# Kernel optimization log

Measured on AMD Instinct MI355X. Metric: run time of the kernel, lower is better.

## Reference

```python
import jax, jax.numpy as jnp
import numpy as np

# Forest of complete binary trees modeling query plans.
B = 512          # number of plans (trees)
D = 11           # tree depth; leaves at level D-1
LEAVES = 1 << (D - 1)      # 1024 leaves per tree
N_INT = LEAVES - 1         # 1023 internal nodes per tree (BFS heap order)
F_LEAF = 64      # leaf ('Scan') feature dim
F_INT = 32       # internal operator feature dim
H = 128          # hidden_dim
NHID = 4         # num_layers=5 -> input layer + 4 hidden layers
DV = 32          # data_vec_dim
OUT = 1 + DV     # latency + data vector


def _mlp(x, W_in, b_in, W_hid, b_hid, W_out, b_out):
    """GenericUnit: Linear+ReLU input layer, NHID Linear+ReLU hidden layers, linear output."""
    h = jax.nn.relu(x @ W_in + b_in)
    for i in range(W_hid.shape[0]):  # small fixed loop over layers
        h = jax.nn.relu(h @ W_hid[i] + b_hid[i])
    return h @ W_out + b_out


def setup_inputs() -> dict:
    key = jax.random.key(0)
    ks = jax.random.split(key, 8)

    def w(k, shape, fan_in):
        return jax.random.normal(k, shape, jnp.float32) * np.float32(1.0 / np.sqrt(fan_in))

    return {
        "leaf_feat": jax.random.normal(ks[0], (B, LEAVES, F_LEAF), jnp.float32),
        "int_feat": jax.random.normal(ks[1], (B, N_INT, F_INT), jnp.float32),
        # leaf unit (0 children)
        "leaf_W_in": w(ks[2], (F_LEAF, H), F_LEAF),
        "leaf_b_in": jnp.zeros((H,), jnp.float32),
        "leaf_W_hid": w(ks[3], (NHID, H, H), H),
        "leaf_b_hid": jnp.zeros((NHID, H), jnp.float32),
        "leaf_W_out": w(ks[4], (H, OUT), H),
        "leaf_b_out": jnp.zeros((OUT,), jnp.float32),
        # internal unit (2 children): input = F_INT + 2*OUT = 98
        "int_W_in": w(ks[5], (F_INT + 2 * OUT, H), F_INT + 2 * OUT),
        "int_b_in": jnp.zeros((H,), jnp.float32),
        "int_W_hid": w(ks[6], (NHID, H, H), H),
        "int_b_hid": jnp.zeros((NHID, H), jnp.float32),
        "int_W_out": w(ks[7], (H, OUT), H),
        "int_b_out": jnp.zeros((OUT,), jnp.float32),
    }


def reference(leaf_feat, int_feat,
              leaf_W_in, leaf_b_in, leaf_W_hid, leaf_b_hid, leaf_W_out, leaf_b_out,
              int_W_in, int_b_in, int_W_hid, int_b_hid, int_W_out, int_b_out):
    # Leaves (level D-1): [B, LEAVES, OUT]
    cur = _mlp(leaf_feat, leaf_W_in, leaf_b_in, leaf_W_hid, leaf_b_hid, leaf_W_out, leaf_b_out)
    # Bottom-up over internal levels; level d has 2^d nodes at BFS offsets [2^d-1, 2^(d+1)-1)
    for d in range(D - 2, -1, -1):
        n = 1 << d
        feats = int_feat[:, n - 1: 2 * n - 1, :]            # [B, n, F_INT]
        children = cur.reshape(B, n, 2 * OUT)               # concat of two child outputs
        unit_in = jnp.concatenate([feats, children], axis=-1)
        cur = _mlp(unit_in, int_W_in, int_b_in, int_W_hid, int_b_hid, int_W_out, int_b_out)
    # Root output, latency channel: [B]
    return cur[:, 0, 0]
```

## Files before the change

kernel.cpp:

```cpp
#include <hip/hip_runtime.h>
#include <cstdint>
#include <cstddef>

constexpr int Bn     = 512;
constexpr int Dd     = 11;
constexpr int LEAVES = 1024;
constexpr int NINT   = 1023;
constexpr int FLEAF  = 64;
constexpr int FINT   = 32;
constexpr int Hh     = 128;
constexpr int OUTC   = 33;

#define THREADS 256
constexpr int KSTR  = 136;
constexpr int MATSZ = 128 * KSTR;

using short8 = __attribute__((ext_vector_type(8))) short;
using f32x4  = __attribute__((ext_vector_type(4))) float;

__device__ __forceinline__ unsigned int f2bf_rne_u(float f) {
  unsigned int u = __float_as_uint(f);
  u += 0x7fffu + ((u >> 16) & 1);
  return u;
}
__device__ __forceinline__ unsigned short f2bf_rne(float f) {
  return (unsigned short)(f2bf_rne_u(f) >> 16);
}
__device__ __forceinline__ float bf2f(unsigned short h) {
  return __uint_as_float((unsigned int)h << 16);
}
__device__ __forceinline__ float trunc_bf(float a) {
  return __uint_as_float(__float_as_uint(a) & 0xffff0000u);
}
__device__ __forceinline__ unsigned int pack_hi_trunc(float a, float b) {
  return (__float_as_uint(a) >> 16) | (__float_as_uint(b) & 0xffff0000u);
}
__device__ __forceinline__ unsigned int pack_lo_rne(float a, float b) {
  return (f2bf_rne_u(a) >> 16) | (f2bf_rne_u(b) & 0xffff0000u);
}

template <int KC, int MT>
__device__ __forceinline__ void dense_layer(
    unsigned short* Ah, unsigned short* Al,
    const unsigned short* __restrict__ WTh, const unsigned short* __restrict__ WTl,
    const float* __restrict__ bias)
{
  const int tid  = threadIdx.x;
  const int wave = tid >> 6;
  const int lane = tid & 63;
  const int quad = lane >> 4;
  const int l16  = lane & 15;
  const int nbase = wave * 32;

  short8 wh[2][KC];
#pragma unroll
  for (int nt = 0; nt < 2; ++nt) {
    const int n = nbase + nt * 16 + l16;
#pragma unroll
    for (int kc = 0; kc < KC; ++kc)
      wh[nt][kc] = *(const short8*)&WTh[n * KSTR + kc * 32 + quad * 8];
  }
  float4 bv[2];
#pragma unroll
  for (int nt = 0; nt < 2; ++nt)
    bv[nt] = *(const float4*)&bias[nbase + nt * 16 + quad * 4];

  f32x4 c[MT][2];
#pragma unroll
  for (int mt = 0; mt < MT; ++mt)
#pragma unroll
    for (int nt = 0; nt < 2; ++nt) c[mt][nt] = (f32x4){0.f, 0.f, 0.f, 0.f};

#pragma unroll
  for (int kc = 0; kc < KC; ++kc) {
    const int k0 = kc * 32 + quad * 8;
    short8 wl[2];
#pragma unroll
    for (int nt = 0; nt < 2; ++nt) {
      const int n = nbase + nt * 16 + l16;
      wl[nt] = *(const short8*)&WTl[n * KSTR + k0];
    }
    short8 ah[MT], al[MT];
#pragma unroll
    for (int mt = 0; mt < MT; ++mt) {
      ah[mt] = *(const short8*)&Ah[(mt * 16 + l16) * KSTR + k0];
      al[mt] = *(const short8*)&Al[(mt * 16 + l16) * KSTR + k0];
    }
#pragma unroll
    for (int mt = 0; mt < MT; ++mt)
#pragma unroll
      for (int nt = 0; nt < 2; ++nt)
        c[mt][nt] = __builtin_amdgcn_mfma_f32_16x16x32_bf16(wh[nt][kc], ah[mt], c[mt][nt], 0, 0, 0);
#pragma unroll
    for (int mt = 0; mt < MT; ++mt)
#pragma unroll
      for (int nt = 0; nt < 2; ++nt)
        c[mt][nt] = __builtin_amdgcn_mfma_f32_16x16x32_bf16(wh[nt][kc], al[mt], c[mt][nt], 0, 0, 0);
#pragma unroll
    for (int mt = 0; mt < MT; ++mt)
#pragma unroll
      for (int nt = 0; nt < 2; ++nt)
        c[mt][nt] = __builtin_amdgcn_mfma_f32_16x16x32_bf16(wl[nt], ah[mt], c[mt][nt], 0, 0, 0);
  }
  __syncthreads();

#pragma unroll
  for (int mt = 0; mt < MT; ++mt) {
    const int m = mt * 16 + l16;
#pragma unroll
    for (int nt = 0; nt < 2; ++nt) {
      const int nb = nbase + nt * 16 + quad * 4;
      float v0 = fmaxf(c[mt][nt][0] + bv[nt].x, 0.f);
      float v1 = fmaxf(c[mt][nt][1] + bv[nt].y, 0.f);
      float v2 = fmaxf(c[mt][nt][2] + bv[nt].z, 0.f);
      float v3 = fmaxf(c[mt][nt][3] + bv[nt].w, 0.f);
      const unsigned int h0 = pack_hi_trunc(v0, v1);
      const unsigned int h1 = pack_hi_trunc(v2, v3);
      const unsigned int l0 = pack_lo_rne(v0 - trunc_bf(v0), v1 - trunc_bf(v1));
      const unsigned int l1 = pack_lo_rne(v2 - trunc_bf(v2), v3 - trunc_bf(v3));
      *(uint2*)&Ah[m * KSTR + nb] = make_uint2(h0, h1);
      *(uint2*)&Al[m * KSTR + nb] = make_uint2(l0, l1);
    }
  }
  __syncthreads();
}

template <int MT>
__device__ __forceinline__ void out_layer(
    const unsigned short* Ah, const unsigned short* Al,
    const unsigned short* __restrict__ WTh, const unsigned short* __restrict__ WTl,
    const float* __restrict__ bias,
    unsigned short* outH, unsigned short* outL, float* finalOut)
{
  const int tid  = threadIdx.x;
  const int wave = tid >> 6;
  const int lane = tid & 63;
  const int quad = lane >> 4;
  const int l16  = lane & 15;
  if (wave < 3) {
    const int n_row = wave * 16 + l16;
    short8 wh[4], wl[4];
#pragma unroll
    for (int kc = 0; kc < 4; ++kc) {
      wh[kc] = *(const short8*)&WTh[n_row * KSTR + kc * 32 + quad * 8];
      wl[kc] = *(const short8*)&WTl[n_row * KSTR + kc * 32 + quad * 8];
    }
    const int nb = wave * 16 + quad * 4;
    const float4 bv = *(const float4*)&bias[nb];
    const float bvr[4] = {bv.x, bv.y, bv.z, bv.w};

    f32x4 c[MT];
#pragma unroll
    for (int mt = 0; mt < MT; ++mt) c[mt] = (f32x4){0.f, 0.f, 0.f, 0.f};
#pragma unroll
    for (int kc = 0; kc < 4; ++kc) {
      const int k0 = kc * 32 + quad * 8;
#pragma unroll
      for (int mt = 0; mt < MT; ++mt) {
        const short8 ah = *(const short8*)&Ah[(mt * 16 + l16) * KSTR + k0];
        const short8 al = *(const short8*)&Al[(mt * 16 + l16) * KSTR + k0];
        c[mt] = __builtin_amdgcn_mfma_f32_16x16x32_bf16(wh[kc], ah, c[mt], 0, 0, 0);
        c[mt] = __builtin_amdgcn_mfma_f32_16x16x32_bf16(wh[kc], al, c[mt], 0, 0, 0);
        c[mt] = __builtin_amdgcn_mfma_f32_16x16x32_bf16(wl[kc], ah, c[mt], 0, 0, 0);
      }
    }
#pragma unroll
    for (int mt = 0; mt < MT; ++mt) {
      const int m = mt * 16 + l16;
#pragma unroll
      for (int r = 0; r < 4; ++r) {
        const int n = nb + r;
        const float v = c[mt][r] + bvr[r];
        if (n < OUTC) {
          outH[m * 33 + n] = (unsigned short)(__float_as_uint(v) >> 16);
          outL[m * 33 + n] = f2bf_rne(v - trunc_bf(v));
        }
        if (finalOut && n == 0 && m == 0) *finalOut = v;
      }
    }
  }
}

__global__ __launch_bounds__(THREADS, 4)
void leaf_kernel(const float* __restrict__ X,
                 const unsigned short* __restrict__ warena,
                 const float* __restrict__ barena,
                 unsigned short* __restrict__ outH, unsigned short* __restrict__ outL)
{
  __shared__ unsigned short Ah[64 * KSTR];
  __shared__ unsigned short Al[64 * KSTR];
  const int row_base = blockIdx.x * 64;
  const int tid = threadIdx.x;

  for (int e = tid; e < 64 * 16; e += THREADS) {
    const int r  = e >> 4;
    const int k0 = (e & 15) << 2;
    const float4 v = *(const float4*)&X[(size_t)(row_base + r) * FLEAF + k0];
    const unsigned int h0 = pack_hi_trunc(v.x, v.y);
    const unsigned int h1 = pack_hi_trunc(v.z, v.w);
    const unsigned int l0 = pack_lo_rne(v.x - trunc_bf(v.x), v.y - trunc_bf(v.y));
    const unsigned int l1 = pack_lo_rne(v.z - trunc_bf(v.z), v.w - trunc_bf(v.w));
    *(uint2*)&Ah[r * KSTR + k0] = make_uint2(h0, h1);
    *(uint2*)&Al[r * KSTR + k0] = make_uint2(l0, l1);
  }
  __syncthreads();

  dense_layer<2, 4>(Ah, Al, warena + 0 * 2 * MATSZ, warena + 0 * 2 * MATSZ + MATSZ, barena + 0 * 128);
#pragma unroll
  for (int l = 0; l < 4; ++l) {
    const int id = 1 + l;
    dense_layer<4, 4>(Ah, Al, warena + id * 2 * MATSZ, warena + id * 2 * MATSZ + MATSZ, barena + id * 128);
  }
  out_layer<4>(Ah, Al, warena + 5 * 2 * MATSZ, warena + 5 * 2 * MATSZ + MATSZ, barena + 5 * 128,
               outH + (size_t)row_base * 33, outL + (size_t)row_base * 33, nullptr);
}

__global__ __launch_bounds__(THREADS, 4)
void int_kernel(const float* __restrict__ feat,
                const unsigned short* __restrict__ prevH, const unsigned short* __restrict__ prevL,
                const unsigned short* __restrict__ warena, const float* __restrict__ barena,
                unsigned short* __restrict__ outH, unsigned short* __restrict__ outL,
                int n, int logn)
{
  __shared__ unsigned short Ah[64 * KSTR];
  __shared__ unsigned short Al[64 * KSTR];
  const int tid = threadIdx.x;
  const int m = tid & 63;
  const int g = tid >> 6;
  const int row = blockIdx.x * 64 + m;
  const int b = row >> logn;
  const int i = row & (n - 1);

  const float* fr = feat + ((size_t)b * NINT + (n - 1) + i) * FINT;
#pragma unroll
  for (int j = 0; j < 4; ++j) {
    const int cch = g + 4 * j;
    const float2 v = *(const float2*)&fr[cch * 2];
    *(unsigned int*)&Ah[m * KSTR + cch * 2] = pack_hi_trunc(v.x, v.y);
    *(unsigned int*)&Al[m * KSTR + cch * 2] = pack_lo_rne(v.x - trunc_bf(v.x), v.y - trunc_bf(v.y));
  }
  const size_t c0 = ((size_t)b * (n << 1) + (i << 1)) * 33;
#pragma unroll
  for (int j = 0; j < 9; ++j) {
    const int p = g + 4 * j;
    if (p < 33) {
      const unsigned int hv = *(const unsigned int*)&prevH[c0 + 2 * p];
      const unsigned int lv = *(const unsigned int*)&prevL[c0 + 2 * p];
      *(unsigned int*)&Ah[m * KSTR + 32 + 2 * p] = hv;
      *(unsigned int*)&Al[m * KSTR + 32 + 2 * p] = lv;
    }
  }
#pragma unroll
  for (int j = 0; j < 4; ++j) {
    const int p = g + 4 * j;
    if (p < 15) {
      *(unsigned int*)&Ah[m * KSTR + 98 + 2 * p] = 0u;
      *(unsigned int*)&Al[m * KSTR + 98 + 2 * p] = 0u;
    }
  }
  __syncthreads();

  dense_layer<4, 4>(Ah, Al, warena + 6 * 2 * MATSZ, warena + 6 * 2 * MATSZ + MATSZ, barena + 6 * 128);
#pragma unroll
  for (int l = 0; l < 4; ++l) {
    const int id = 7 + l;
    dense_layer<4, 4>(Ah, Al, warena + id * 2 * MATSZ, warena + id * 2 * MATSZ + MATSZ, barena + id * 128);
  }
  out_layer<4>(Ah, Al, warena + 11 * 2 * MATSZ, warena + 11 * 2 * MATSZ + MATSZ, barena + 11 * 128,
               outH + (size_t)blockIdx.x * 64 * 33, outL + (size_t)blockIdx.x * 64 * 33, nullptr);
}

__global__ __launch_bounds__(THREADS, 4)
void tail_kernel(const float* __restrict__ feat,
                 const unsigned short* __restrict__ g6H, const unsigned short* __restrict__ g6L,
                 const unsigned short* __restrict__ warena, const float* __restrict__ barena,
                 float* __restrict__ out)
{
  __shared__ unsigned short Ah[64 * KSTR];
  __shared__ unsigned short Al[64 * KSTR];
  __shared__ unsigned short oH[64 * 33];
  __shared__ unsigned short oL[64 * 33];
  const int tid = threadIdx.x;
  const int m = tid & 63;
  const int g = tid >> 6;
  const int b = blockIdx.x;

  for (int d = 5; d >= 0; --d) {
    const int n = 1 << d;
    const int i = m & (n - 1);
    const float* fr = feat + ((size_t)b * NINT + (n - 1) + i) * FINT;
#pragma unroll
    for (int j = 0; j < 4; ++j) {
      const int cch = g + 4 * j;
      const float2 v = *(const float2*)&fr[cch * 2];
      *(unsigned int*)&Ah[m * KSTR + cch * 2] = pack_hi_trunc(v.x, v.y);
      *(unsigned int*)&Al[m * KSTR + cch * 2] = pack_lo_rne(v.x - trunc_bf(v.x), v.y - trunc_bf(v.y));
    }
    const unsigned short* sH;
    const unsigned short* sL;
    size_t c0;
    if (d == 5) { sH = g6H; sL = g6L; c0 = ((size_t)b * 64 + 2 * i) * 33; }
    else        { sH = oH;  sL = oL;  c0 = (size_t)(2 * i) * 33; }
#pragma unroll
    for (int j = 0; j < 9; ++j) {
      const int p = g + 4 * j;
      if (p < 33) {
        const unsigned int hv = *(const unsigned int*)&sH[c0 + 2 * p];
        const unsigned int lv = *(const unsigned int*)&sL[c0 + 2 * p];
        *(unsigned int*)&Ah[m * KSTR + 32 + 2 * p] = hv;
        *(unsigned int*)&Al[m * KSTR + 32 + 2 * p] = lv;
      }
    }
#pragma unroll
    for (int j = 0; j < 4; ++j) {
      const int p = g + 4 * j;
      if (p < 15) {
        *(unsigned int*)&Ah[m * KSTR + 98 + 2 * p] = 0u;
        *(unsigned int*)&Al[m * KSTR + 98 + 2 * p] = 0u;
      }
    }
    __syncthreads();

    if (d == 5) {
      dense_layer<4, 2>(Ah, Al, warena + 6 * 2 * MATSZ, warena + 6 * 2 * MATSZ + MATSZ, barena + 6 * 128);
#pragma unroll
      for (int l = 0; l < 4; ++l) {
        const int id = 7 + l;
        dense_layer<4, 2>(Ah, Al, warena + id * 2 * MATSZ, warena + id * 2 * MATSZ + MATSZ, barena + id * 128);
      }
      out_layer<2>(Ah, Al, warena + 11 * 2 * MATSZ, warena + 11 * 2 * MATSZ + MATSZ, barena + 11 * 128,
                   oH, oL, nullptr);
    } else {
      dense_layer<4, 1>(Ah, Al, warena + 6 * 2 * MATSZ, warena + 6 * 2 * MATSZ + MATSZ, barena + 6 * 128);
#pragma unroll
      for (int l = 0; l < 4; ++l) {
        const int id = 7 + l;
        dense_layer<4, 1>(Ah, Al, warena + id * 2 * MATSZ, warena + id * 2 * MATSZ + MATSZ, barena + id * 128);
      }
      out_layer<1>(Ah, Al, warena + 11 * 2 * MATSZ, warena + 11 * 2 * MATSZ + MATSZ, barena + 11 * 128,
                   oH, oL, (d == 0) ? (out + b) : nullptr);
    }
    __syncthreads();
  }
}

__global__ void prep_kernel(const float* __restrict__ lW_in, const float* __restrict__ lW_hid,
                            const float* __restrict__ lW_out, const float* __restrict__ lb_in,
                            const float* __restrict__ lb_hid, const float* __restrict__ lb_out,
                            const float* __restrict__ iW_in, const float* __restrict__ iW_hid,
                            const float* __restrict__ iW_out, const float* __restrict__ ib_in,
                            const float* __restrict__ ib_hid, const float* __restrict__ ib_out,
                            unsigned short* __restrict__ warena, float* __restrict__ barena)
{
  const int id = blockIdx.y;
  const float* W; const float* bs; int K, N;
  if (id == 0)       { W = lW_in;                        bs = lb_in;                 K = FLEAF; N = Hh; }
  else if (id <= 4)  { W = lW_hid + (id - 1) * Hh * Hh;  bs = lb_hid + (id - 1) * Hh; K = Hh;   N = Hh; }
  else if (id == 5)  { W = lW_out;                       bs = lb_out;                K = Hh;    N = OUTC; }
  else if (id == 6)  { W = iW_in;                        bs = ib_in;                 K = FINT + 2 * OUTC; N = Hh; }
  else if (id <= 10) { W = iW_hid + (id - 7) * Hh * Hh;  bs = ib_hid + (id - 7) * Hh; K = Hh;   N = Hh; }
  else               { W = iW_out;                       bs = ib_out;                K = Hh;    N = OUTC; }

  unsigned short* dh = warena + id * 2 * MATSZ;
  unsigned short* dl = dh + MATSZ;
  const int e = blockIdx.x * THREADS + threadIdx.x;
  if (e < MATSZ) {
    const int nn = e / KSTR;
    const int kk = e - nn * KSTR;
    const float v = (kk < K && nn < N) ? W[(size_t)kk * N + nn] : 0.f;
    const unsigned short h = f2bf_rne(v);
    dh[e] = h;
    dl[e] = f2bf_rne(v - bf2f(h));
  }
  if (blockIdx.x == 0 && threadIdx.x < 128)
    barena[id * 128 + threadIdx.x] = (threadIdx.x < N) ? bs[threadIdx.x] : 0.f;
}

extern "C" void kernel_launch(void* const* d_in, const int* in_sizes, int n_in,
                              void* d_out, int out_size, void* d_ws, size_t ws_size,
                              hipStream_t stream) {
  const float* leaf_feat = (const float*)d_in[0];
  const float* int_feat  = (const float*)d_in[1];
  const float* lW_in  = (const float*)d_in[2];
  const float* lb_in  = (const float*)d_in[3];
  const float* lW_hid = (const float*)d_in[4];
  const float* lb_hid = (const float*)d_in[5];
  const float* lW_out = (const float*)d_in[6];
  const float* lb_out = (const float*)d_in[7];
  const float* iW_in  = (const float*)d_in[8];
  const float* ib_in  = (const float*)d_in[9];
  const float* iW_hid = (const float*)d_in[10];
  const float* ib_hid = (const float*)d_in[11];
  const float* iW_out = (const float*)d_in[12];
  const float* ib_out = (const float*)d_in[13];
  float* out = (float*)d_out;

  const size_t rowsA = (size_t)Bn * LEAVES;
  const size_t rowsB = rowsA / 2;
  unsigned short* AH = (unsigned short*)d_ws;
  unsigned short* AL = AH + rowsA * 33;
  unsigned short* BH = AL + rowsA * 33;
  unsigned short* BL = BH + rowsB * 33;
  unsigned short* warena = BL + rowsB * 33;
  float* barena = (float*)(warena + 24 * MATSZ);

  prep_kernel<<<dim3((MATSZ + THREADS - 1) / THREADS, 12), THREADS, 0, stream>>>(
      lW_in, lW_hid, lW_out, lb_in, lb_hid, lb_out,
      iW_in, iW_hid, iW_out, ib_in, ib_hid, ib_out, warena, barena);

  leaf_kernel<<<(Bn * LEAVES) / 64, THREADS, 0, stream>>>(leaf_feat, warena, barena, AH, AL);

  int_kernel<<<4096, THREADS, 0, stream>>>(int_feat, AH, AL, warena, barena, BH, BL, 512, 9);
  int_kernel<<<2048, THREADS, 0, stream>>>(int_feat, BH, BL, warena, barena, AH, AL, 256, 8);
  int_kernel<<<1024, THREADS, 0, stream>>>(int_feat, AH, AL, warena, barena, BH, BL, 128, 7);
  int_kernel<<< 512, THREADS, 0, stream>>>(int_feat, BH, BL, warena, barena, AH, AL,  64, 6);

  tail_kernel<<<Bn, THREADS, 0, stream>>>(int_feat, AH, AL, warena, barena, out);
}
```

Measured before the change: 913.7 us.

## Use 128-row tiles, 2x2 wave grid, and fragment-ordered weight layout

Doubles the row tile per block to 128 and splits the four waves into a 2x2 grid over rows and output columns, so each weight fragment loaded from global memory feeds more MFMAs. The prep kernel now stores weights pre-swizzled in MFMA fragment order, making each lane's weight load one contiguous 16-byte read. Staging loops are flattened and the tail kernel uses a 32-row tile. In exchange, register and LDS use per block go up and the occupancy hint drops to 2 blocks, and the later levels launch fewer blocks.

```diff
diff --git a/kernel.cpp b/kernel.cpp
--- a/kernel.cpp
+++ b/kernel.cpp
@@ -2,18 +2,16 @@
 #include <cstdint>
 #include <cstddef>
 
-constexpr int Bn     = 512;
-constexpr int Dd     = 11;
-constexpr int LEAVES = 1024;
-constexpr int NINT   = 1023;
-constexpr int FLEAF  = 64;
-constexpr int FINT   = 32;
-constexpr int Hh     = 128;
-constexpr int OUTC   = 33;
+constexpr int Bn    = 512;
+constexpr int NINT  = 1023;
+constexpr int FLEAF = 64;
+constexpr int FINT  = 32;
+constexpr int Hh    = 128;
+constexpr int OUTC  = 33;
 
 #define THREADS 256
 constexpr int KSTR  = 136;
-constexpr int MATSZ = 128 * KSTR;
+constexpr int MATSZ = 16384;
 
 using short8 = __attribute__((ext_vector_type(8))) short;
 using f32x4  = __attribute__((ext_vector_type(4))) float;
@@ -39,77 +37,78 @@
   return (f2bf_rne_u(a) >> 16) | (f2bf_rne_u(b) & 0xffff0000u);
 }
 
+__device__ __forceinline__ const short8* wfrag(const unsigned short* W, int ntg, int kc, int lane) {
+  return (const short8*)&W[(((ntg << 2) + kc) << 6 | lane) << 3];
+}
+
 template <int KC, int MT>
 __device__ __forceinline__ void dense_layer(
     unsigned short* Ah, unsigned short* Al,
-    const unsigned short* __restrict__ WTh, const unsigned short* __restrict__ WTl,
+    const unsigned short* __restrict__ Wh, const unsigned short* __restrict__ Wl,
     const float* __restrict__ bias)
 {
   const int tid  = threadIdx.x;
   const int wave = tid >> 6;
+  const int wn   = wave & 1;
+  const int wm   = wave >> 1;
   const int lane = tid & 63;
   const int quad = lane >> 4;
   const int l16  = lane & 15;
-  const int nbase = wave * 32;
-
-  short8 wh[2][KC];
-#pragma unroll
-  for (int nt = 0; nt < 2; ++nt) {
-    const int n = nbase + nt * 16 + l16;
+  const int mbase = wm * MT * 16;
+
+  short8 wh[4][KC];
+#pragma unroll
+  for (int nt = 0; nt < 4; ++nt)
 #pragma unroll
     for (int kc = 0; kc < KC; ++kc)
-      wh[nt][kc] = *(const short8*)&WTh[n * KSTR + kc * 32 + quad * 8];
-  }
-  float4 bv[2];
-#pragma unroll
-  for (int nt = 0; nt < 2; ++nt)
-    bv[nt] = *(const float4*)&bias[nbase + nt * 16 + quad * 4];
-
-  f32x4 c[MT][2];
+      wh[nt][kc] = *wfrag(Wh, wn * 4 + nt, kc, lane);
+  float4 bv[4];
+#pragma unroll
+  for (int nt = 0; nt < 4; ++nt)
+    bv[nt] = *(const float4*)&bias[wn * 64 + nt * 16 + quad * 4];
+
+  f32x4 c[MT][4];
 #pragma unroll
   for (int mt = 0; mt < MT; ++mt)
 #pragma unroll
-    for (int nt = 0; nt < 2; ++nt) c[mt][nt] = (f32x4){0.f, 0.f, 0.f, 0.f};
+    for (int nt = 0; nt < 4; ++nt) c[mt][nt] = (f32x4){0.f, 0.f, 0.f, 0.f};
 
 #pragma unroll
   for (int kc = 0; kc < KC; ++kc) {
     const int k0 = kc * 32 + quad * 8;
-    short8 wl[2];
-#pragma unroll
-    for (int nt = 0; nt < 2; ++nt) {
-      const int n = nbase + nt * 16 + l16;
-      wl[nt] = *(const short8*)&WTl[n * KSTR + k0];
-    }
+    short8 wl[4];
+#pragma unroll
+    for (int nt = 0; nt < 4; ++nt) wl[nt] = *wfrag(Wl, wn * 4 + nt, kc, lane);
     short8 ah[MT], al[MT];
 #pragma unroll
     for (int mt = 0; mt < MT; ++mt) {
-      ah[mt] = *(const short8*)&Ah[(mt * 16 + l16) * KSTR + k0];
-      al[mt] = *(const short8*)&Al[(mt * 16 + l16) * KSTR + k0];
+      ah[mt] = *(const short8*)&Ah[(mbase + mt * 16 + l16) * KSTR + k0];
+      al[mt] = *(const short8*)&Al[(mbase + mt * 16 + l16) * KSTR + k0];
     }
 #pragma unroll
     for (int mt = 0; mt < MT; ++mt)
 #pragma unroll
-      for (int nt = 0; nt < 2; ++nt)
+      for (int nt = 0; nt < 4; ++nt)
         c[mt][nt] = __builtin_amdgcn_mfma_f32_16x16x32_bf16(wh[nt][kc], ah[mt], c[mt][nt], 0, 0, 0);
 #pragma unroll
     for (int mt = 0; mt < MT; ++mt)
 #pragma unroll
-      for (int nt = 0; nt < 2; ++nt)
+      for (int nt = 0; nt < 4; ++nt)
         c[mt][nt] = __builtin_amdgcn_mfma_f32_16x16x32_bf16(wh[nt][kc], al[mt], c[mt][nt], 0, 0, 0);
 #pragma unroll
     for (int mt = 0; mt < MT; ++mt)
 #pragma unroll
-      for (int nt = 0; nt < 2; ++nt)
+      for (int nt = 0; nt < 4; ++nt)
         c[mt][nt] = __builtin_amdgcn_mfma_f32_16x16x32_bf16(wl[nt], ah[mt], c[mt][nt], 0, 0, 0);
   }
   __syncthreads();
 
 #pragma unroll
   for (int mt = 0; mt < MT; ++mt) {
-    const int m = mt * 16 + l16;
-#pragma unroll
-    for (int nt = 0; nt < 2; ++nt) {
-      const int nb = nbase + nt * 16 + quad * 4;
+    const int m = mbase + mt * 16 + l16;
+#pragma unroll
+    for (int nt = 0; nt < 4; ++nt) {
+      const int nb = wn * 64 + nt * 16 + quad * 4;
       float v0 = fmaxf(c[mt][nt][0] + bv[nt].x, 0.f);
       float v1 = fmaxf(c[mt][nt][1] + bv[nt].y, 0.f);
       float v2 = fmaxf(c[mt][nt][2] + bv[nt].z, 0.f);
@@ -128,45 +127,46 @@
 template <int MT>
 __device__ __forceinline__ void out_layer(
     const unsigned short* Ah, const unsigned short* Al,
-    const unsigned short* __restrict__ WTh, const unsigned short* __restrict__ WTl,
+    const unsigned short* __restrict__ Wh, const unsigned short* __restrict__ Wl,
     const float* __restrict__ bias,
     unsigned short* outH, unsigned short* outL, float* finalOut)
 {
   const int tid  = threadIdx.x;
   const int wave = tid >> 6;
+  const int wn   = wave & 1;
+  const int wm   = wave >> 1;
   const int lane = tid & 63;
   const int quad = lane >> 4;
   const int l16  = lane & 15;
-  if (wave < 3) {
-    const int n_row = wave * 16 + l16;
-    short8 wh[4], wl[4];
-#pragma unroll
-    for (int kc = 0; kc < 4; ++kc) {
-      wh[kc] = *(const short8*)&WTh[n_row * KSTR + kc * 32 + quad * 8];
-      wl[kc] = *(const short8*)&WTl[n_row * KSTR + kc * 32 + quad * 8];
-    }
-    const int nb = wave * 16 + quad * 4;
-    const float4 bv = *(const float4*)&bias[nb];
-    const float bvr[4] = {bv.x, bv.y, bv.z, bv.w};
-
+  const int mbase = wm * MT * 16;
+
+#pragma unroll
+  for (int nt = 0; nt < 2; ++nt) {
+    const int ntg = wn * 2 + nt;
+    if (ntg >= 3) continue;
     f32x4 c[MT];
 #pragma unroll
     for (int mt = 0; mt < MT; ++mt) c[mt] = (f32x4){0.f, 0.f, 0.f, 0.f};
 #pragma unroll
     for (int kc = 0; kc < 4; ++kc) {
       const int k0 = kc * 32 + quad * 8;
+      const short8 bwh = *wfrag(Wh, ntg, kc, lane);
+      const short8 bwl = *wfrag(Wl, ntg, kc, lane);
 #pragma unroll
       for (int mt = 0; mt < MT; ++mt) {
-        const short8 ah = *(const short8*)&Ah[(mt * 16 + l16) * KSTR + k0];
-        const short8 al = *(const short8*)&Al[(mt * 16 + l16) * KSTR + k0];
-        c[mt] = __builtin_amdgcn_mfma_f32_16x16x32_bf16(wh[kc], ah, c[mt], 0, 0, 0);
-        c[mt] = __builtin_amdgcn_mfma_f32_16x16x32_bf16(wh[kc], al, c[mt], 0, 0, 0);
-        c[mt] = __builtin_amdgcn_mfma_f32_16x16x32_bf16(wl[kc], ah, c[mt], 0, 0, 0);
+        const short8 ah = *(const short8*)&Ah[(mbase + mt * 16 + l16) * KSTR + k0];
+        const short8 al = *(const short8*)&Al[(mbase + mt * 16 + l16) * KSTR + k0];
+        c[mt] = __builtin_amdgcn_mfma_f32_16x16x32_bf16(bwh, ah, c[mt], 0, 0, 0);
+        c[mt] = __builtin_amdgcn_mfma_f32_16x16x32_bf16(bwh, al, c[mt], 0, 0, 0);
+        c[mt] = __builtin_amdgcn_mfma_f32_16x16x32_bf16(bwl, ah, c[mt], 0, 0, 0);
       }
     }
+    const int nb = ntg * 16 + quad * 4;
+    const float4 bvv = *(const float4*)&bias[nb];
+    const float bvr[4] = {bvv.x, bvv.y, bvv.z, bvv.w};
 #pragma unroll
     for (int mt = 0; mt < MT; ++mt) {
-      const int m = mt * 16 + l16;
+      const int m = mbase + mt * 16 + l16;
 #pragma unroll
       for (int r = 0; r < 4; ++r) {
         const int n = nb + r;
@@ -181,18 +181,18 @@
   }
 }
 
-__global__ __launch_bounds__(THREADS, 4)
+__global__ __launch_bounds__(THREADS, 2)
 void leaf_kernel(const float* __restrict__ X,
                  const unsigned short* __restrict__ warena,
                  const float* __restrict__ barena,
                  unsigned short* __restrict__ outH, unsigned short* __restrict__ outL)
 {
-  __shared__ unsigned short Ah[64 * KSTR];
-  __shared__ unsigned short Al[64 * KSTR];
-  const int row_base = blockIdx.x * 64;
+  __shared__ unsigned short Ah[128 * KSTR];
+  __shared__ unsigned short Al[128 * KSTR];
+  const int row_base = blockIdx.x * 128;
   const int tid = threadIdx.x;
 
-  for (int e = tid; e < 64 * 16; e += THREADS) {
+  for (int e = tid; e < 128 * 16; e += THREADS) {
     const int r  = e >> 4;
     const int k0 = (e & 15) << 2;
     const float4 v = *(const float4*)&X[(size_t)(row_base + r) * FLEAF + k0];
@@ -207,139 +207,97 @@
 
   dense_layer<2, 4>(Ah, Al, warena + 0 * 2 * MATSZ, warena + 0 * 2 * MATSZ + MATSZ, barena + 0 * 128);
 #pragma unroll
-  for (int l = 0; l < 4; ++l) {
-    const int id = 1 + l;
-    dense_layer<4, 4>(Ah, Al, warena + id * 2 * MATSZ, warena + id * 2 * MATSZ + MATSZ, barena + id * 128);
-  }
+  for (int l = 1; l <= 4; ++l)
+    dense_layer<4, 4>(Ah, Al, warena + l * 2 * MATSZ, warena + l * 2 * MATSZ + MATSZ, barena + l * 128);
   out_layer<4>(Ah, Al, warena + 5 * 2 * MATSZ, warena + 5 * 2 * MATSZ + MATSZ, barena + 5 * 128,
                outH + (size_t)row_base * 33, outL + (size_t)row_base * 33, nullptr);
 }
 
-__global__ __launch_bounds__(THREADS, 4)
+__global__ __launch_bounds__(THREADS, 2)
 void int_kernel(const float* __restrict__ feat,
                 const unsigned short* __restrict__ prevH, const unsigned short* __restrict__ prevL,
                 const unsigned short* __restrict__ warena, const float* __restrict__ barena,
                 unsigned short* __restrict__ outH, unsigned short* __restrict__ outL,
                 int n, int logn)
 {
-  __shared__ unsigned short Ah[64 * KSTR];
-  __shared__ unsigned short Al[64 * KSTR];
+  __shared__ unsigned short Ah[128 * KSTR];
+  __shared__ unsigned short Al[128 * KSTR];
   const int tid = threadIdx.x;
-  const int m = tid & 63;
-  const int g = tid >> 6;
-  const int row = blockIdx.x * 64 + m;
-  const int b = row >> logn;
-  const int i = row & (n - 1);
-
-  const float* fr = feat + ((size_t)b * NINT + (n - 1) + i) * FINT;
-#pragma unroll
-  for (int j = 0; j < 4; ++j) {
-    const int cch = g + 4 * j;
-    const float2 v = *(const float2*)&fr[cch * 2];
-    *(unsigned int*)&Ah[m * KSTR + cch * 2] = pack_hi_trunc(v.x, v.y);
-    *(unsigned int*)&Al[m * KSTR + cch * 2] = pack_lo_rne(v.x - trunc_bf(v.x), v.y - trunc_bf(v.y));
-  }
-  const size_t c0 = ((size_t)b * (n << 1) + (i << 1)) * 33;
-#pragma unroll
-  for (int j = 0; j < 9; ++j) {
-    const int p = g + 4 * j;
-    if (p < 33) {
-      const unsigned int hv = *(const unsigned int*)&prevH[c0 + 2 * p];
-      const unsigned int lv = *(const unsigned int*)&prevL[c0 + 2 * p];
-      *(unsigned int*)&Ah[m * KSTR + 32 + 2 * p] = hv;
-      *(unsigned int*)&Al[m * KSTR + 32 + 2 * p] = lv;
-    }
-  }
-#pragma unroll
-  for (int j = 0; j < 4; ++j) {
-    const int p = g + 4 * j;
-    if (p < 15) {
-      *(unsigned int*)&Ah[m * KSTR + 98 + 2 * p] = 0u;
-      *(unsigned int*)&Al[m * KSTR + 98 + 2 * p] = 0u;
+  const int row0 = blockIdx.x * 128;
+
+  for (int e = tid; e < 128 * 64; e += THREADS) {
+    const int m = e >> 6;
+    const int c = e & 63;
+    const int row = row0 + m;
+    const int b = row >> logn;
+    const int i = row & (n - 1);
+    if (c < 16) {
+      const float2 v = *(const float2*)&feat[((size_t)b * NINT + (n - 1) + i) * FINT + 2 * c];
+      *(unsigned int*)&Ah[m * KSTR + 2 * c] = pack_hi_trunc(v.x, v.y);
+      *(unsigned int*)&Al[m * KSTR + 2 * c] = pack_lo_rne(v.x - trunc_bf(v.x), v.y - trunc_bf(v.y));
+    } else if (c < 49) {
+      const int p = c - 16;
+      const size_t c0 = ((size_t)b * (n << 1) + (i << 1)) * 33;
+      *(unsigned int*)&Ah[m * KSTR + 32 + 2 * p] = *(const unsigned int*)&prevH[c0 + 2 * p];
+      *(unsigned int*)&Al[m * KSTR + 32 + 2 * p] = *(const unsigned int*)&prevL[c0 + 2 * p];
+    } else {
+      const int z = c - 49;
+      *(unsigned int*)&Ah[m * KSTR + 98 + 2 * z] = 0u;
+      *(unsigned int*)&Al[m * KSTR + 98 + 2 * z] = 0u;
     }
   }
   __syncthreads();
 
-  dense_layer<4, 4>(Ah, Al, warena + 6 * 2 * MATSZ, warena + 6 * 2 * MATSZ + MATSZ, barena + 6 * 128);
-#pragma unroll
-  for (int l = 0; l < 4; ++l) {
-    const int id = 7 + l;
-    dense_layer<4, 4>(Ah, Al, warena + id * 2 * MATSZ, warena + id * 2 * MATSZ + MATSZ, barena + id * 128);
-  }
+#pragma unroll
+  for (int l = 6; l <= 10; ++l)
+    dense_layer<4, 4>(Ah, Al, warena + l * 2 * MATSZ, warena + l * 2 * MATSZ + MATSZ, barena + l * 128);
   out_layer<4>(Ah, Al, warena + 11 * 2 * MATSZ, warena + 11 * 2 * MATSZ + MATSZ, barena + 11 * 128,
-               outH + (size_t)blockIdx.x * 64 * 33, outL + (size_t)blockIdx.x * 64 * 33, nullptr);
-}
-
-__global__ __launch_bounds__(THREADS, 4)
+               outH + (size_t)row0 * 33, outL + (size_t)row0 * 33, nullptr);
+}
+
+__global__ __launch_bounds__(THREADS, 2)
 void tail_kernel(const float* __restrict__ feat,
                  const unsigned short* __restrict__ g6H, const unsigned short* __restrict__ g6L,
                  const unsigned short* __restrict__ warena, const float* __restrict__ barena,
                  float* __restrict__ out)
 {
-  __shared__ unsigned short Ah[64 * KSTR];
-  __shared__ unsigned short Al[64 * KSTR];
-  __shared__ unsigned short oH[64 * 33];
-  __shared__ unsigned short oL[64 * 33];
+  __shared__ unsigned short Ah[32 * KSTR];
+  __shared__ unsigned short Al[32 * KSTR];
+  __shared__ unsigned short oH[32 * 33];
+  __shared__ unsigned short oL[32 * 33];
   const int tid = threadIdx.x;
-  const int m = tid & 63;
-  const int g = tid >> 6;
   const int b = blockIdx.x;
 
   for (int d = 5; d >= 0; --d) {
     const int n = 1 << d;
-    const int i = m & (n - 1);
-    const float* fr = feat + ((size_t)b * NINT + (n - 1) + i) * FINT;
-#pragma unroll
-    for (int j = 0; j < 4; ++j) {
-      const int cch = g + 4 * j;
-      const float2 v = *(const float2*)&fr[cch * 2];
-      *(unsigned int*)&Ah[m * KSTR + cch * 2] = pack_hi_trunc(v.x, v.y);
-      *(unsigned int*)&Al[m * KSTR + cch * 2] = pack_lo_rne(v.x - trunc_bf(v.x), v.y - trunc_bf(v.y));
-    }
-    const unsigned short* sH;
-    const unsigned short* sL;
-    size_t c0;
-    if (d == 5) { sH = g6H; sL = g6L; c0 = ((size_t)b * 64 + 2 * i) * 33; }
-    else        { sH = oH;  sL = oL;  c0 = (size_t)(2 * i) * 33; }
-#pragma unroll
-    for (int j = 0; j < 9; ++j) {
-      const int p = g + 4 * j;
-      if (p < 33) {
-        const unsigned int hv = *(const unsigned int*)&sH[c0 + 2 * p];
-        const unsigned int lv = *(const unsigned int*)&sL[c0 + 2 * p];
-        *(unsigned int*)&Ah[m * KSTR + 32 + 2 * p] = hv;
-        *(unsigned int*)&Al[m * KSTR + 32 + 2 * p] = lv;
+    for (int e = tid; e < 32 * 64; e += THREADS) {
+      const int m = e >> 6;
+      const int c = e & 63;
+      const int i = m & (n - 1);
+      if (c < 16) {
+        const float2 v = *(const float2*)&feat[((size_t)b * NINT + (n - 1) + i) * FINT + 2 * c];
+        *(unsigned int*)&Ah[m * KSTR + 2 * c] = pack_hi_trunc(v.x, v.y);
+        *(unsigned int*)&Al[m * KSTR + 2 * c] = pack_lo_rne(v.x - trunc_bf(v.x), v.y - trunc_bf(v.y));
+      } else if (c < 49) {
+        const int p = c - 16;
+        const unsigned short* sH = (d == 5) ? g6H : oH;
+        const unsigned short* sL = (d == 5) ? g6L : oL;
+        const size_t c0 = (d == 5) ? ((size_t)b * 64 + 2 * i) * 33 : (size_t)(2 * i) * 33;
+        *(unsigned int*)&Ah[m * KSTR + 32 + 2 * p] = *(const unsigned int*)&sH[c0 + 2 * p];
+        *(unsigned int*)&Al[m * KSTR + 32 + 2 * p] = *(const unsigned int*)&sL[c0 + 2 * p];
+      } else {
+        const int z = c - 49;
+        *(unsigned int*)&Ah[m * KSTR + 98 + 2 * z] = 0u;
+        *(unsigned int*)&Al[m * KSTR + 98 + 2 * z] = 0u;
       }
     }
-#pragma unroll
-    for (int j = 0; j < 4; ++j) {
-      const int p = g + 4 * j;
-      if (p < 15) {
-        *(unsigned int*)&Ah[m * KSTR + 98 + 2 * p] = 0u;
-        *(unsigned int*)&Al[m * KSTR + 98 + 2 * p] = 0u;
-      }
-    }
     __syncthreads();
 
-    if (d == 5) {
-      dense_layer<4, 2>(Ah, Al, warena + 6 * 2 * MATSZ, warena + 6 * 2 * MATSZ + MATSZ, barena + 6 * 128);
-#pragma unroll
-      for (int l = 0; l < 4; ++l) {
-        const int id = 7 + l;
-        dense_layer<4, 2>(Ah, Al, warena + id * 2 * MATSZ, warena + id * 2 * MATSZ + MATSZ, barena + id * 128);
-      }
-      out_layer<2>(Ah, Al, warena + 11 * 2 * MATSZ, warena + 11 * 2 * MATSZ + MATSZ, barena + 11 * 128,
-                   oH, oL, nullptr);
-    } else {
-      dense_layer<4, 1>(Ah, Al, warena + 6 * 2 * MATSZ, warena + 6 * 2 * MATSZ + MATSZ, barena + 6 * 128);
-#pragma unroll
-      for (int l = 0; l < 4; ++l) {
-        const int id = 7 + l;
-        dense_layer<4, 1>(Ah, Al, warena + id * 2 * MATSZ, warena + id * 2 * MATSZ + MATSZ, barena + id * 128);
-      }
-      out_layer<1>(Ah, Al, warena + 11 * 2 * MATSZ, warena + 11 * 2 * MATSZ + MATSZ, barena + 11 * 128,
-                   oH, oL, (d == 0) ? (out + b) : nullptr);
-    }
+#pragma unroll
+    for (int l = 6; l <= 10; ++l)
+      dense_layer<4, 1>(Ah, Al, warena + l * 2 * MATSZ, warena + l * 2 * MATSZ + MATSZ, barena + l * 128);
+    out_layer<1>(Ah, Al, warena + 11 * 2 * MATSZ, warena + 11 * 2 * MATSZ + MATSZ, barena + 11 * 128,
+                 oH, oL, (d == 0) ? (out + b) : nullptr);
     __syncthreads();
   }
 }
@@ -354,19 +312,25 @@
 {
   const int id = blockIdx.y;
   const float* W; const float* bs; int K, N;
-  if (id == 0)       { W = lW_in;                        bs = lb_in;                 K = FLEAF; N = Hh; }
-  else if (id <= 4)  { W = lW_hid + (id - 1) * Hh * Hh;  bs = lb_hid + (id - 1) * Hh; K = Hh;   N = Hh; }
-  else if (id == 5)  { W = lW_out;                       bs = lb_out;                K = Hh;    N = OUTC; }
-  else if (id == 6)  { W = iW_in;                        bs = ib_in;                 K = FINT + 2 * OUTC; N = Hh; }
-  else if (id <= 10) { W = iW_hid + (id - 7) * Hh * Hh;  bs = ib_hid + (id - 7) * Hh; K = Hh;   N = Hh; }
-  else               { W = iW_out;                       bs = ib_out;                K = Hh;    N = OUTC; }
+  if (id == 0)       { W = lW_in;                       bs = lb_in;                  K = FLEAF; N = Hh; }
+  else if (id <= 4)  { W = lW_hid + (id - 1) * Hh * Hh; bs = lb_hid + (id - 1) * Hh; K = Hh;    N = Hh; }
+  else if (id == 5)  { W = lW_out;                      bs = lb_out;                 K = Hh;    N = OUTC; }
+  else if (id == 6)  { W = iW_in;                       bs = ib_in;                  K = FINT + 2 * OUTC; N = Hh; }
+  else if (id <= 10) { W = iW_hid + (id - 7) * Hh * Hh; bs = ib_hid + (id - 7) * Hh; K = Hh;    N = Hh; }
+  else               { W = iW_out;                      bs = ib_out;                 K = Hh;    N = OUTC; }
 
   unsigned short* dh = warena + id * 2 * MATSZ;
   unsigned short* dl = dh + MATSZ;
   const int e = blockIdx.x * THREADS + threadIdx.x;
   if (e < MATSZ) {
-    const int nn = e / KSTR;
-    const int kk = e - nn * KSTR;
+    const int ntg  = e >> 11;
+    const int kc   = (e >> 9) & 3;
+    const int lane = (e >> 3) & 63;
+    const int j    = e & 7;
+    const int quad = lane >> 4;
+    const int l16  = lane & 15;
+    const int nn = ntg * 16 + l16;
+    const int kk = kc * 32 + quad * 8 + j;
     const float v = (kk < K && nn < N) ? W[(size_t)kk * N + nn] : 0.f;
     const unsigned short h = f2bf_rne(v);
     dh[e] = h;
@@ -395,7 +359,7 @@
   const float* ib_out = (const float*)d_in[13];
   float* out = (float*)d_out;
 
-  const size_t rowsA = (size_t)Bn * LEAVES;
+  const size_t rowsA = (size_t)Bn * 1024;
   const size_t rowsB = rowsA / 2;
   unsigned short* AH = (unsigned short*)d_ws;
   unsigned short* AL = AH + rowsA * 33;
@@ -404,16 +368,16 @@
   unsigned short* warena = BL + rowsB * 33;
   float* barena = (float*)(warena + 24 * MATSZ);
 
-  prep_kernel<<<dim3((MATSZ + THREADS - 1) / THREADS, 12), THREADS, 0, stream>>>(
+  prep_kernel<<<dim3(MATSZ / THREADS, 12), THREADS, 0, stream>>>(
       lW_in, lW_hid, lW_out, lb_in, lb_hid, lb_out,
       iW_in, iW_hid, iW_out, ib_in, ib_hid, ib_out, warena, barena);
 
-  leaf_kernel<<<(Bn * LEAVES) / 64, THREADS, 0, stream>>>(leaf_feat, warena, barena, AH, AL);
-
-  int_kernel<<<4096, THREADS, 0, stream>>>(int_feat, AH, AL, warena, barena, BH, BL, 512, 9);
-  int_kernel<<<2048, THREADS, 0, stream>>>(int_feat, BH, BL, warena, barena, AH, AL, 256, 8);
-  int_kernel<<<1024, THREADS, 0, stream>>>(int_feat, AH, AL, warena, barena, BH, BL, 128, 7);
-  int_kernel<<< 512, THREADS, 0, stream>>>(int_feat, BH, BL, warena, barena, AH, AL,  64, 6);
+  leaf_kernel<<<(Bn * 1024) / 128, THREADS, 0, stream>>>(leaf_feat, warena, barena, AH, AL);
+
+  int_kernel<<<2048, THREADS, 0, stream>>>(int_feat, AH, AL, warena, barena, BH, BL, 512, 9);
+  int_kernel<<<1024, THREADS, 0, stream>>>(int_feat, BH, BL, warena, barena, AH, AL, 256, 8);
+  int_kernel<<< 512, THREADS, 0, stream>>>(int_feat, AH, AL, warena, barena, BH, BL, 128, 7);
+  int_kernel<<< 256, THREADS, 0, stream>>>(int_feat, BH, BL, warena, barena, AH, AL,  64, 6);
 
   tail_kernel<<<Bn, THREADS, 0, stream>>>(int_feat, AH, AL, warena, barena, out);
 }
```

Result: slower. 1.502 ms (+64.4%).
